# Kernel tuning notes

Hardware: AMD Instinct MI355X
Metric: run time of the kernel (lower is better)

Reference implementation:

```python
import jax, jax.numpy as jnp
import numpy as np

D = 64        # kg_embedding_dim
T = 4096      # tokens
N = 20000     # kg nodes
M = T + N     # total nodes
E = 100000    # edges
R = 50        # relation types (num_edge_embeddings)
V = 100000    # num_node_embeddings
TOK = 768     # token_embedding_size


def setup_inputs() -> dict:
    key = jax.random.key(0)
    ks = jax.random.split(key, 24)
    s = 0.05
    node_ids = jax.random.randint(ks[0], (N,), 0, V)
    edge_index = jax.random.randint(ks[1], (2, E), 0, M)
    rel_ids = jax.random.randint(ks[2], (E,), 0, R)
    edge_attr = jax.nn.one_hot(rel_ids, R, dtype=jnp.float32)  # [E,R]
    token_embeddings = jax.random.normal(ks[3], (T, TOK), dtype=jnp.float32)
    node_type_labels = jax.random.randint(ks[4], (M,), 0, 3)
    return {
        'node_ids': node_ids,
        'edge_index': edge_index,
        'edge_attr': edge_attr,
        'token_embeddings': token_embeddings,
        'node_type_labels': node_type_labels,
        # learned params
        'kg_emb': jax.random.normal(ks[5], (V, D), dtype=jnp.float32) * s,
        'rel_emb': jax.random.normal(ks[6], (R, D), dtype=jnp.float32) * s,
        'w_e2': jax.random.normal(ks[7], (D, D * D), dtype=jnp.float32) * s,
        'b_e2': jnp.zeros((D * D,), dtype=jnp.float32),
        'att1_w': jax.random.normal(ks[8], (2 * D, 1), dtype=jnp.float32) * s,
        'att1_b': jnp.zeros((1,), dtype=jnp.float32),
        'root1': jax.random.normal(ks[9], (D, D), dtype=jnp.float32) * s,
        'bias1': jnp.zeros((D,), dtype=jnp.float32),
        'att2_w': jax.random.normal(ks[10], (2 * D, 1), dtype=jnp.float32) * s,
        'att2_b': jnp.zeros((1,), dtype=jnp.float32),
        'root2': jax.random.normal(ks[11], (D, D), dtype=jnp.float32) * s,
        'bias2': jnp.zeros((D,), dtype=jnp.float32),
        'w_lin1': jax.random.normal(ks[12], (TOK, D), dtype=jnp.float32) * s,
        'b_lin1': jnp.zeros((D,), dtype=jnp.float32),
        'w_lin2': jax.random.normal(ks[13], (D, TOK), dtype=jnp.float32) * s,
        'b_lin2': jnp.zeros((TOK,), dtype=jnp.float32),
        'w_nt': jax.random.normal(ks[14], (D, 3), dtype=jnp.float32) * s,
        'b_nt': jnp.zeros((3,), dtype=jnp.float32),
    }


def _ecgat(x, src, dst, w_edge, att_w, att_b, root, bias):
    # x: [M,D], w_edge: [E,D,D]
    x_j = x[src]                                    # gather source nodes [E,D]
    x_i = x[dst]                                    # gather target nodes [E,D]
    nbr = jnp.einsum('ed,edo->eo', x_j, w_edge)     # per-edge matmul [E,D]
    a = jnp.concatenate([x_i, nbr], axis=1) @ att_w + att_b   # [E,1]
    a = jax.nn.softmax(a, axis=0)                   # global softmax over edges (dim=0 in torch)
    msg = x_j * a                                   # message = x_j * alpha
    aggr = jax.ops.segment_sum(msg, dst, num_segments=M)      # scatter-add [M,D]
    return aggr + x @ root + bias


def reference(node_ids, edge_index, edge_attr, token_embeddings, node_type_labels,
              kg_emb, rel_emb, w_e2, b_e2,
              att1_w, att1_b, root1, bias1,
              att2_w, att2_b, root2, bias2,
              w_lin1, b_lin1, w_lin2, b_lin2, w_nt, b_nt):
    src, dst = edge_index[0], edge_index[1]
    tok = token_embeddings @ w_lin1 + b_lin1        # [T,D]
    nodes = kg_emb[node_ids]                        # [N,D]
    x = jnp.concatenate([tok, nodes], axis=0)       # [M,D]

    # EdgeNet (shared by both conv layers, same edge_attr -> compute once)
    e_emb = edge_attr @ rel_emb                     # [E,D]
    w_edge = jax.nn.relu(e_emb @ w_e2 + b_e2).reshape(E, D, D)  # [E,D,D]

    x1 = _ecgat(x, src, dst, w_edge, att1_w, att1_b, root1, bias1)
    h = jax.nn.relu(x1)                             # dropout = identity in eval
    final_x = _ecgat(h, src, dst, w_edge, att2_w, att2_b, root2, bias2)

    # link_pred loss (MSE, masked, mean over all elements)
    pred_tails = final_x[src] + e_emb
    edge_labels = final_x[dst]
    mask = (edge_attr[:, -3:].sum(axis=1) == 0).astype(final_x.dtype)[:, None]
    kge_loss = jnp.mean((pred_tails - edge_labels) ** 2 * mask)

    # node-type classification loss (cross entropy)
    logp = jax.nn.log_softmax(final_x @ w_nt + b_nt, axis=-1)
    nt_loss = -jnp.mean(jnp.take_along_axis(logp, node_type_labels[:, None], axis=1))

    final_outputs = final_x @ w_lin2 + b_lin2       # [M,TOK]
    return final_outputs, kge_loss, nt_loss
```

## Files before the change

kernel.cpp:

```cpp
#include <hip/hip_runtime.h>

#define Dd   64
#define Tt   4096
#define Nn   20000
#define Mm   24096
#define Ee   100000
#define Rr   50
#define TOK  768

#define NB_TOK   512
#define NB_NODES 1250
#define NB_RELID 4883
#define NB_W     800
#define NB_ZERO  95
#define NBM_HIST 391
#define NBM_U    13
#define NBM_P    6024
#define NBA_FILL 391
#define NBA_ATT  2048

__device__ __forceinline__ float waveRed(float v){
  #pragma unroll
  for(int o=32;o;o>>=1) v += __shfl_xor(v,o,64);
  return v;
}

__global__ __launch_bounds__(256) void k_prep(
    const float* __restrict__ A, const float* __restrict__ wl1, const float* __restrict__ bl1,
    const int* __restrict__ ids, const float* __restrict__ kg,
    const float* __restrict__ ea, int* __restrict__ relid,
    const float* __restrict__ rel, const float* __restrict__ w2, const float* __restrict__ b2,
    float* __restrict__ W, int* __restrict__ deg, float* __restrict__ S,
    float* __restrict__ x){
  __shared__ float As[8*TOK];
  int b = blockIdx.x;
  const int t = threadIdx.x, lane = t&63, wave = t>>6;
  if(b < NB_TOK){
    const int rbase = b*8;
    #pragma unroll
    for(int i=0;i<6;i++){
      int f = t + 256*i;
      int row = f/192, c4 = (f - row*192)*4;
      *(float4*)&As[row*TOK + c4] = *(const float4*)&A[(size_t)(rbase+row)*TOK + c4];
    }
    __syncthreads();
    const int r0 = wave*2, r1 = r0+1;
    float a0=bl1[lane], a1=a0, c0=0.f, c1=0.f;
    for(int k=0;k<TOK;k+=2){
      float w0 = wl1[(size_t)k*Dd + lane];
      float w1 = wl1[(size_t)(k+1)*Dd + lane];
      a0 += As[r0*TOK+k]*w0;  c0 += As[r0*TOK+k+1]*w1;
      a1 += As[r1*TOK+k]*w0;  c1 += As[r1*TOK+k+1]*w1;
    }
    x[(size_t)(rbase+r0)*Dd + lane] = a0+c0;
    x[(size_t)(rbase+r1)*Dd + lane] = a1+c1;
  } else if(b < NB_TOK+NB_NODES){
    int tt = (b-NB_TOK)*256 + t;
    int i = tt>>4, c = tt&15;
    ((float4*)x)[(size_t)(Tt+i)*16 + c] = ((const float4*)kg)[(size_t)ids[i]*16 + c];
  } else if(b < NB_TOK+NB_NODES+NB_RELID){
    int tt = (b-NB_TOK-NB_NODES)*256 + t;
    size_t g4 = (size_t)tt*4;
    if(g4 < (size_t)Ee*Rr){
      float4 v = *(const float4*)&ea[g4];
      #pragma unroll
      for(int j=0;j<4;j++){
        if(((const float*)&v)[j] > 0.5f){
          unsigned g = (unsigned)(g4 + j);
          unsigned e = g / 50u;
          relid[e] = (int)(g - e*50u);
        }
      }
    }
  } else if(b < NB_TOK+NB_NODES+NB_RELID+NB_W){
    int tt = (b-NB_TOK-NB_NODES-NB_RELID)*256 + t;
    int r = tt>>12, j = tt&4095;
    float acc = b2[j];
    const float* rp = rel + r*Dd;
    #pragma unroll 8
    for(int d=0;d<Dd;d++) acc += rp[d] * w2[(size_t)d*4096 + j];
    W[tt] = acc > 0.f ? acc : 0.f;
  } else {
    int tt = (b-NB_TOK-NB_NODES-NB_RELID-NB_W)*256 + t;
    if(tt < Mm) deg[tt] = 0;
    else if(tt < Mm+4) S[tt-Mm] = 0.f;
  }
}

__global__ __launch_bounds__(256) void k_mid(const int* __restrict__ ei,
    int* __restrict__ deg, const float* __restrict__ W,
    const float* __restrict__ a1w, const float* __restrict__ a2w,
    float* __restrict__ U1, float* __restrict__ U2,
    const float* __restrict__ x, float* __restrict__ p){
  int b = blockIdx.x;
  const int t = threadIdx.x, lane = t&63, wave = t>>6;
  if(b < NBM_HIST){
    int e = b*256 + t;
    if(e < Ee) atomicAdd(&deg[ei[Ee+e]], 1);
  } else if(b < NBM_HIST+NBM_U){
    int tt = (b-NBM_HIST)*256 + t;
    if(tt < Rr*Dd){
      const float* wp = W + (size_t)(tt>>6)*4096 + (size_t)(tt&63)*Dd;
      float s1 = 0.f, s2 = 0.f;
      #pragma unroll 8
      for(int o=0;o<Dd;o++){ float w = wp[o]; s1 += w*a1w[Dd+o]; s2 += w*a2w[Dd+o]; }
      U1[tt] = s1; U2[tt] = s2;
    }
  } else {
    int i = (b-NBM_HIST-NBM_U)*4 + wave;
    float pv = waveRed(x[(size_t)i*Dd + lane] * a1w[lane]);
    if(lane==0) p[i] = pv;
  }
}

__global__ __launch_bounds__(1024) void k_scan(const int* __restrict__ deg,
    int* __restrict__ rowptr, int* __restrict__ cursor){
  __shared__ int ts[1024];
  int t = threadIdx.x;
  int base = t*24;
  int loc[24];
  int s = 0;
  #pragma unroll
  for(int j=0;j<24;j++){
    int idx = base+j;
    int d = (idx < Mm) ? deg[idx] : 0;
    loc[j] = s; s += d;
  }
  ts[t] = s;
  __syncthreads();
  for(int off=1; off<1024; off<<=1){
    int add = (t>=off) ? ts[t-off] : 0;
    __syncthreads();
    ts[t] += add;
    __syncthreads();
  }
  int excl = ts[t] - s;
  #pragma unroll
  for(int j=0;j<24;j++){
    int idx = base+j;
    if(idx < Mm){ int v = excl + loc[j]; rowptr[idx] = v; cursor[idx] = v; }
  }
  if(t==1023) rowptr[Mm] = ts[1023];
}

__global__ __launch_bounds__(256) void k_attf(const float* __restrict__ x,
    const int* __restrict__ ei, const int* __restrict__ relid,
    const float* __restrict__ U, const float* __restrict__ p,
    const float* __restrict__ ab, float* __restrict__ expa, float* __restrict__ S,
    int* __restrict__ cursor, int* __restrict__ eidx,
    int dorelu, int dofill){
  __shared__ float sw[4];
  int b = blockIdx.x;
  if(dofill){
    if(b < NBA_FILL){
      int e = b*256 + threadIdx.x;
      if(e < Ee){
        int d = ei[Ee+e];
        int pos = atomicAdd(&cursor[d], 1);
        eidx[pos] = e;
      }
      return;
    }
    b -= NBA_FILL;
  }
  int lane = threadIdx.x&63, wid = threadIdx.x>>6;
  int gw = b*4 + wid;
  float ab0 = ab[0];
  float acc = 0.f;
  for(int e = gw; e < Ee; e += 4*NBA_ATT){
    int src = ei[e], dst = ei[Ee+e], r = relid[e];
    float xv = x[(size_t)src*Dd + lane];
    if(dorelu) xv = fmaxf(xv, 0.f);
    float v = waveRed(xv * U[r*Dd + lane]);
    float ex = expf(v + p[dst] + ab0);
    if(lane==0) expa[e] = ex;
    acc += ex;
  }
  if(lane==0) sw[wid] = acc;
  __syncthreads();
  if(threadIdx.x==0) atomicAdd(S, sw[0]+sw[1]+sw[2]+sw[3]);
}

__global__ __launch_bounds__(256) void k_aggr(const float* __restrict__ x,
    const int* __restrict__ ei, const int* __restrict__ rowptr,
    const int* __restrict__ eidx, const float* __restrict__ expa,
    const float* __restrict__ S, const float* __restrict__ root,
    const float* __restrict__ bias, const float* __restrict__ awn,
    float* __restrict__ y, float* __restrict__ pnext, int dorelu){
  int lane = threadIdx.x&63, wid = threadIdx.x>>6;
  int dst = blockIdx.x*4 + wid;
  float invS = 1.f / S[0];
  int j0 = rowptr[dst], j1 = rowptr[dst+1];
  float acc = 0.f;
  for(int j=j0; j<j1; j++){
    int e = eidx[j];
    float a = expa[e];
    int src = ei[e];
    float xv = x[(size_t)src*Dd + lane];
    if(dorelu) xv = fmaxf(xv, 0.f);
    acc += a*xv;
  }
  acc *= invS;
  float xd = x[(size_t)dst*Dd + lane];
  if(dorelu) xd = fmaxf(xd, 0.f);
  float rsum = bias[lane];
  #pragma unroll 16
  for(int k=0;k<Dd;k++){
    float xk = __shfl(xd, k, 64);
    rsum += xk * root[k*Dd + lane];
  }
  float o = acc + rsum;
  y[(size_t)dst*Dd + lane] = o;
  if(pnext){
    float orl = fmaxf(o, 0.f);
    float pv = waveRed(orl * awn[lane]);
    if(lane==0) pnext[dst] = pv;
  }
}

__global__ void k_loss(const float* __restrict__ fx, const int* __restrict__ ei,
    const int* __restrict__ relid, const float* __restrict__ rel,
    const int* __restrict__ lab, const float* __restrict__ wnt,
    const float* __restrict__ bnt, float* __restrict__ S){
  __shared__ float sr[4];
  if(blockIdx.x < 512){
    int wid = threadIdx.x>>6, lane = threadIdx.x&63;
    int gw = blockIdx.x*4 + wid;
    float acc = 0.f;
    for(int e=gw; e<Ee; e+=2048){
      int r = relid[e];
      if(r < 47){
        int src = ei[e], dst = ei[Ee+e];
        float d = fx[(size_t)src*Dd + lane] + rel[r*Dd + lane] - fx[(size_t)dst*Dd + lane];
        acc += d*d;
      }
    }
    acc = waveRed(acc);
    if(lane==0) sr[wid] = acc;
    __syncthreads();
    if(threadIdx.x==0) atomicAdd(&S[2], sr[0]+sr[1]+sr[2]+sr[3]);
  } else {
    int nb = blockIdx.x - 512;
    int i = nb*256 + threadIdx.x;
    float contrib = 0.f;
    if(i < Mm){
      const float* r = fx + (size_t)i*Dd;
      float l0 = bnt[0], l1 = bnt[1], l2 = bnt[2];
      #pragma unroll 8
      for(int k=0;k<Dd;k++){
        float f = r[k];
        l0 += f*wnt[k*3+0]; l1 += f*wnt[k*3+1]; l2 += f*wnt[k*3+2];
      }
      float mx = fmaxf(l0, fmaxf(l1,l2));
      float lse = logf(expf(l0-mx)+expf(l1-mx)+expf(l2-mx)) + mx;
      int lb = lab[i];
      float lp = (lb==0 ? l0 : (lb==1 ? l1 : l2)) - lse;
      contrib = -lp;
    }
    float s = waveRed(contrib);
    if((threadIdx.x&63)==0) sr[threadIdx.x>>6] = s;
    __syncthreads();
    if(threadIdx.x==0) atomicAdd(&S[3], sr[0]+sr[1]+sr[2]+sr[3]);
  }
}

__global__ __launch_bounds__(256) void k_out(const float* __restrict__ fx,
    const float* __restrict__ w, const float* __restrict__ b,
    const float* __restrict__ S, float* __restrict__ out){
  if(blockIdx.x==0 && blockIdx.y==0 && threadIdx.x==0){
    size_t base = (size_t)Mm*TOK;
    out[base+0] = S[2] / (float)(Ee*Dd);
    out[base+1] = S[3] / (float)Mm;
  }
  __shared__ float aT[Dd][36];
  __shared__ float ws[Dd][128];
  const int t = threadIdx.x;
  const int r0 = blockIdx.x*32, co = blockIdx.y*128;
  #pragma unroll
  for(int i=0;i<2;i++){
    int f = t + 256*i;
    int r = f>>4, k4 = (f&15)*4;
    float4 v = *(const float4*)&fx[(size_t)(r0+r)*Dd + k4];
    aT[k4+0][r]=v.x; aT[k4+1][r]=v.y; aT[k4+2][r]=v.z; aT[k4+3][r]=v.w;
  }
  #pragma unroll
  for(int i=0;i<8;i++){
    int f = t + 256*i;
    int kk = f>>5, c4 = (f&31)*4;
    *(float4*)&ws[kk][c4] = *(const float4*)&w[(size_t)kk*TOK + co + c4];
  }
  __syncthreads();
  const int tr = t>>5, tc = t&31;
  const int rb = tr*4, cb = tc*4;
  float4 bv = *(const float4*)&b[co+cb];
  float acc[4][4];
  #pragma unroll
  for(int i=0;i<4;i++){ acc[i][0]=bv.x; acc[i][1]=bv.y; acc[i][2]=bv.z; acc[i][3]=bv.w; }
  #pragma unroll 8
  for(int k=0;k<Dd;k++){
    float4 a  = *(const float4*)&aT[k][rb];
    float4 wv = *(const float4*)&ws[k][cb];
    #pragma unroll
    for(int i=0;i<4;i++){
      float av = ((const float*)&a)[i];
      acc[i][0] += av*wv.x; acc[i][1] += av*wv.y;
      acc[i][2] += av*wv.z; acc[i][3] += av*wv.w;
    }
  }
  #pragma unroll
  for(int i=0;i<4;i++){
    float4 o; o.x=acc[i][0]; o.y=acc[i][1]; o.z=acc[i][2]; o.w=acc[i][3];
    *(float4*)&out[(size_t)(r0+rb+i)*TOK + co + cb] = o;
  }
}

extern "C" void kernel_launch(void* const* d_in, const int* in_sizes, int n_in,
                              void* d_out, int out_size, void* d_ws, size_t ws_size,
                              hipStream_t stream) {
  const int*   node_ids = (const int*)d_in[0];
  const int*   ei       = (const int*)d_in[1];
  const float* eattr    = (const float*)d_in[2];
  const float* tokemb   = (const float*)d_in[3];
  const int*   labels   = (const int*)d_in[4];
  const float* kg       = (const float*)d_in[5];
  const float* rel      = (const float*)d_in[6];
  const float* w_e2     = (const float*)d_in[7];
  const float* b_e2     = (const float*)d_in[8];
  const float* a1w      = (const float*)d_in[9];
  const float* a1b      = (const float*)d_in[10];
  const float* root1    = (const float*)d_in[11];
  const float* bias1    = (const float*)d_in[12];
  const float* a2w      = (const float*)d_in[13];
  const float* a2b      = (const float*)d_in[14];
  const float* root2    = (const float*)d_in[15];
  const float* bias2    = (const float*)d_in[16];
  const float* wlin1    = (const float*)d_in[17];
  const float* blin1    = (const float*)d_in[18];
  const float* wlin2    = (const float*)d_in[19];
  const float* blin2    = (const float*)d_in[20];
  const float* wnt      = (const float*)d_in[21];
  const float* bnt      = (const float*)d_in[22];

  float* wsb = (float*)d_ws;
  float* x    = wsb;
  float* h    = x  + (size_t)Mm*Dd;
  float* fx   = h  + (size_t)Mm*Dd;
  float* W    = fx + (size_t)Mm*Dd;
  float* U1   = W  + Rr*4096;
  float* U2   = U1 + Rr*Dd;
  float* expa = U2 + Rr*Dd;
  float* p    = expa + Ee;
  float* S    = p + Mm;
  int* relid  = (int*)(S + 4);
  int* deg    = relid + Ee;
  int* rowptr = deg + Mm;
  int* cursor = rowptr + Mm + 1;
  int* eidx   = cursor + Mm;
  float* out  = (float*)d_out;

  k_prep<<<NB_TOK+NB_NODES+NB_RELID+NB_W+NB_ZERO, 256, 0, stream>>>(
      tokemb, wlin1, blin1, node_ids, kg, eattr, relid, rel, w_e2, b_e2, W, deg, S, x);
  k_mid <<<NBM_HIST+NBM_U+NBM_P, 256, 0, stream>>>(ei, deg, W, a1w, a2w, U1, U2, x, p);
  k_scan<<<1, 1024, 0, stream>>>(deg, rowptr, cursor);

  k_attf<<<NBA_FILL+NBA_ATT, 256, 0, stream>>>(x, ei, relid, U1, p, a1b, expa, S,
                                               cursor, eidx, 0, 1);
  k_aggr<<<Mm/4, 256, 0, stream>>>(x, ei, rowptr, eidx, expa, S, root1, bias1, a2w, h, p, 0);

  k_attf<<<NBA_ATT, 256, 0, stream>>>(h, ei, relid, U2, p, a2b, expa, S+1,
                                      (int*)0, (int*)0, 1, 0);
  k_aggr<<<Mm/4, 256, 0, stream>>>(h, ei, rowptr, eidx, expa, S+1, root2, bias2,
                                   (const float*)0, fx, (float*)0, 1);

  k_loss<<<607, 256, 0, stream>>>(fx, ei, relid, rel, labels, wnt, bnt, S);
  dim3 og(Mm/32, TOK/128);
  k_out <<<og, 256, 0, stream>>>(fx, wlin2, blin2, S, out);
}
```

Baseline: 424.6 us.

## Fuse node-type loss into second aggregation and KGE loss into output GEMM

Removes the separate loss kernel. The node-type cross-entropy is now computed inside the second k_aggr, using wave reductions on each output row while it is still in registers. The link-prediction loss runs as extra blocks of the output GEMM kernel, each handling 64 consecutive edges with shuffled indices instead of a strided loop. The last finishing block, found with an atomic counter, writes the final loss scalars. This saves one launch and a full reread of fx for the classification loss, at the cost of extra atomics and a last-block synchronization pattern.

```diff
diff --git a/kernel.cpp b/kernel.cpp
--- a/kernel.cpp
+++ b/kernel.cpp
@@ -18,6 +18,7 @@
 #define NBM_P    6024
 #define NBA_FILL 391
 #define NBA_ATT  2048
+#define NKGE     391
 
 __device__ __forceinline__ float waveRed(float v){
   #pragma unroll
@@ -83,7 +84,7 @@
   } else {
     int tt = (b-NB_TOK-NB_NODES-NB_RELID-NB_W)*256 + t;
     if(tt < Mm) deg[tt] = 0;
-    else if(tt < Mm+4) S[tt-Mm] = 0.f;
+    else if(tt < Mm+8) S[tt-Mm] = 0.f;
   }
 }
 
@@ -186,7 +187,10 @@
     const int* __restrict__ eidx, const float* __restrict__ expa,
     const float* __restrict__ S, const float* __restrict__ root,
     const float* __restrict__ bias, const float* __restrict__ awn,
-    float* __restrict__ y, float* __restrict__ pnext, int dorelu){
+    float* __restrict__ y, float* __restrict__ pnext, int dorelu,
+    const int* __restrict__ lab, const float* __restrict__ wnt,
+    const float* __restrict__ bnt, float* __restrict__ Snt){
+  __shared__ float sn[4];
   int lane = threadIdx.x&63, wid = threadIdx.x>>6;
   int dst = blockIdx.x*4 + wid;
   float invS = 1.f / S[0];
@@ -216,66 +220,71 @@
     float pv = waveRed(orl * awn[lane]);
     if(lane==0) pnext[dst] = pv;
   }
-}
-
-__global__ void k_loss(const float* __restrict__ fx, const int* __restrict__ ei,
-    const int* __restrict__ relid, const float* __restrict__ rel,
-    const int* __restrict__ lab, const float* __restrict__ wnt,
-    const float* __restrict__ bnt, float* __restrict__ S){
-  __shared__ float sr[4];
-  if(blockIdx.x < 512){
-    int wid = threadIdx.x>>6, lane = threadIdx.x&63;
-    int gw = blockIdx.x*4 + wid;
+  if(lab){
+    float l0 = waveRed(o * wnt[lane*3+0]);
+    float l1 = waveRed(o * wnt[lane*3+1]);
+    float l2 = waveRed(o * wnt[lane*3+2]);
+    if(lane==0){
+      l0 += bnt[0]; l1 += bnt[1]; l2 += bnt[2];
+      float mx = fmaxf(l0, fmaxf(l1,l2));
+      float lse = logf(expf(l0-mx)+expf(l1-mx)+expf(l2-mx)) + mx;
+      int lb = lab[dst];
+      float lp = (lb==0 ? l0 : (lb==1 ? l1 : l2)) - lse;
+      sn[wid] = -lp;
+    }
+    __syncthreads();
+    if(threadIdx.x==0) atomicAdd(Snt, sn[0]+sn[1]+sn[2]+sn[3]);
+  }
+}
+
+__global__ __launch_bounds__(256) void k_out(const float* __restrict__ fx,
+    const float* __restrict__ w, const float* __restrict__ b,
+    const int* __restrict__ ei, const int* __restrict__ relid,
+    const float* __restrict__ rel, float* __restrict__ S,
+    float* __restrict__ out){
+  __shared__ float aT[Dd][36];
+  __shared__ float ws[Dd][128];
+  if(blockIdx.x < NKGE){
+    __shared__ float sr[4];
+    const int t = threadIdx.x, lane = t&63, wid = t>>6;
+    const int cb = (blockIdx.x*4 + wid)*64;
+    int e = cb + lane;
+    bool vld = e < Ee;
+    int sv = vld ? ei[e]    : 0;
+    int dv = vld ? ei[Ee+e] : 0;
+    int rv = vld ? relid[e] : 47;
     float acc = 0.f;
-    for(int e=gw; e<Ee; e+=2048){
-      int r = relid[e];
-      if(r < 47){
-        int src = ei[e], dst = ei[Ee+e];
-        float d = fx[(size_t)src*Dd + lane] + rel[r*Dd + lane] - fx[(size_t)dst*Dd + lane];
-        acc += d*d;
-      }
+    #pragma unroll 8
+    for(int j=0;j<64;j++){
+      int r = __shfl(rv, j, 64);
+      int s = __shfl(sv, j, 64);
+      int d = __shfl(dv, j, 64);
+      float m = (r < 47) ? 1.f : 0.f;
+      float diff = fx[(size_t)s*Dd + lane] + rel[r*Dd + lane] - fx[(size_t)d*Dd + lane];
+      acc += m*diff*diff;
     }
     acc = waveRed(acc);
     if(lane==0) sr[wid] = acc;
     __syncthreads();
-    if(threadIdx.x==0) atomicAdd(&S[2], sr[0]+sr[1]+sr[2]+sr[3]);
-  } else {
-    int nb = blockIdx.x - 512;
-    int i = nb*256 + threadIdx.x;
-    float contrib = 0.f;
-    if(i < Mm){
-      const float* r = fx + (size_t)i*Dd;
-      float l0 = bnt[0], l1 = bnt[1], l2 = bnt[2];
-      #pragma unroll 8
-      for(int k=0;k<Dd;k++){
-        float f = r[k];
-        l0 += f*wnt[k*3+0]; l1 += f*wnt[k*3+1]; l2 += f*wnt[k*3+2];
+    if(t==0){
+      atomicAdd(&S[2], sr[0]+sr[1]+sr[2]+sr[3]);
+      __threadfence();
+      int prev = atomicAdd((int*)&S[4], 1);
+      if(prev == NKGE-1){
+        float v2 = atomicAdd(&S[2], 0.f);
+        float v3 = atomicAdd(&S[3], 0.f);
+        size_t base = (size_t)Mm*TOK;
+        out[base+0] = v2 / (float)(Ee*Dd);
+        out[base+1] = v3 / (float)Mm;
       }
-      float mx = fmaxf(l0, fmaxf(l1,l2));
-      float lse = logf(expf(l0-mx)+expf(l1-mx)+expf(l2-mx)) + mx;
-      int lb = lab[i];
-      float lp = (lb==0 ? l0 : (lb==1 ? l1 : l2)) - lse;
-      contrib = -lp;
-    }
-    float s = waveRed(contrib);
-    if((threadIdx.x&63)==0) sr[threadIdx.x>>6] = s;
-    __syncthreads();
-    if(threadIdx.x==0) atomicAdd(&S[3], sr[0]+sr[1]+sr[2]+sr[3]);
-  }
-}
-
-__global__ __launch_bounds__(256) void k_out(const float* __restrict__ fx,
-    const float* __restrict__ w, const float* __restrict__ b,
-    const float* __restrict__ S, float* __restrict__ out){
-  if(blockIdx.x==0 && blockIdx.y==0 && threadIdx.x==0){
-    size_t base = (size_t)Mm*TOK;
-    out[base+0] = S[2] / (float)(Ee*Dd);
-    out[base+1] = S[3] / (float)Mm;
-  }
-  __shared__ float aT[Dd][36];
-  __shared__ float ws[Dd][128];
+    }
+    return;
+  }
+  const int bb = blockIdx.x - NKGE;
+  const int byc = bb / 753;
+  const int bx  = bb - byc*753;
   const int t = threadIdx.x;
-  const int r0 = blockIdx.x*32, co = blockIdx.y*128;
+  const int r0 = bx*32, co = byc*128;
   #pragma unroll
   for(int i=0;i<2;i++){
     int f = t + 256*i;
@@ -351,7 +360,7 @@
   float* expa = U2 + Rr*Dd;
   float* p    = expa + Ee;
   float* S    = p + Mm;
-  int* relid  = (int*)(S + 4);
+  int* relid  = (int*)(S + 8);
   int* deg    = relid + Ee;
   int* rowptr = deg + Mm;
   int* cursor = rowptr + Mm + 1;
@@ -365,14 +374,15 @@
 
   k_attf<<<NBA_FILL+NBA_ATT, 256, 0, stream>>>(x, ei, relid, U1, p, a1b, expa, S,
                                                cursor, eidx, 0, 1);
-  k_aggr<<<Mm/4, 256, 0, stream>>>(x, ei, rowptr, eidx, expa, S, root1, bias1, a2w, h, p, 0);
+  k_aggr<<<Mm/4, 256, 0, stream>>>(x, ei, rowptr, eidx, expa, S, root1, bias1, a2w, h, p, 0,
+                                   (const int*)0, (const float*)0, (const float*)0, (float*)0);
 
   k_attf<<<NBA_ATT, 256, 0, stream>>>(h, ei, relid, U2, p, a2b, expa, S+1,
                                       (int*)0, (int*)0, 1, 0);
   k_aggr<<<Mm/4, 256, 0, stream>>>(h, ei, rowptr, eidx, expa, S+1, root2, bias2,
-                                   (const float*)0, fx, (float*)0, 1);
-
-  k_loss<<<607, 256, 0, stream>>>(fx, ei, relid, rel, labels, wnt, bnt, S);
-  dim3 og(Mm/32, TOK/128);
-  k_out <<<og, 256, 0, stream>>>(fx, wlin2, blin2, S, out);
-}
+                                   (const float*)0, fx, (float*)0, 1,
+                                   labels, wnt, bnt, &S[3]);
+
+  k_out <<<NKGE + (Mm/32)*(TOK/128), 256, 0, stream>>>(
+      fx, wlin2, blin2, ei, relid, rel, S, out);
+}
```

Result: slower. 459.7 us (+8.3%).
